# Optimization experiments

Measured on AMD Instinct MI355X. Metric: run time of the kernel, lower is better.

The kernel has to match this reference:

```python
import jax, jax.numpy as jnp
import numpy as np

B, C, H, W = 512, 256, 7, 7
NS, HS, WS = 16, 14, 14
CK = 128            # key/value channels of the 1x1 convs
REP = 1024          # MLP_HEAD_DIM
IN = 2 * CK * H * W # 12544 = concat(query_value, attended_value) flattened


def setup_inputs() -> dict:
    key = jax.random.key(0)
    ks = jax.random.split(key, 14)
    s = lambda n: 1.0 / np.sqrt(n)
    f32 = jnp.float32
    return {
        "x": jax.random.normal(ks[0], (B, C, H, W), f32),
        "sup_features": jax.random.normal(ks[1], (NS, C, HS, WS), f32),
        # 1x1 conv weights [out_c, in_c] + biases
        "Wqv": jax.random.normal(ks[2], (CK, C), f32) * s(C),
        "bqv": jnp.zeros((CK,), f32),
        "Wqk": jax.random.normal(ks[3], (CK, C), f32) * s(C),
        "bqk": jnp.zeros((CK,), f32),
        "Wsv": jax.random.normal(ks[4], (CK, C), f32) * s(C),
        "bsv": jnp.zeros((CK,), f32),
        "Wsk": jax.random.normal(ks[5], (CK, C), f32) * s(C),
        "bsk": jnp.zeros((CK,), f32),
        # fc layers, torch Linear convention: W [out, in]
        "W6c": jax.random.normal(ks[6], (REP, IN), f32) * s(IN),
        "b6c": jnp.zeros((REP,), f32),
        "W7c": jax.random.normal(ks[7], (REP, REP), f32) * s(REP),
        "b7c": jnp.zeros((REP,), f32),
        "W6r": jax.random.normal(ks[8], (REP, IN), f32) * s(IN),
        "b6r": jnp.zeros((REP,), f32),
        "W7r": jax.random.normal(ks[9], (REP, REP), f32) * s(REP),
        "b7r": jnp.zeros((REP,), f32),
    }


def _conv1x1(w, b, t):
    # 1x1 conv == per-pixel channel mixing
    return jnp.einsum('oc,bchw->bohw', w, t) + b[None, :, None, None]


def reference(x, sup_features, Wqv, bqv, Wqk, bqk, Wsv, bsv, Wsk, bsk,
              W6c, b6c, W7c, b7c, W6r, b6r, W7r, b7r):
    qv = _conv1x1(Wqv, bqv, x)                                          # [B,128,H,W]
    qk = _conv1x1(Wqk, bqk, x).transpose(0, 2, 3, 1).reshape(-1, CK)    # [B*H*W,128]
    sv = _conv1x1(Wsv, bsv, sup_features).transpose(0, 2, 3, 1).reshape(-1, CK)  # [M,128]
    sk = _conv1x1(Wsk, bsk, sup_features).transpose(1, 0, 2, 3).reshape(CK, -1)  # [128,M]
    sim = jax.nn.softmax(qk @ sk, axis=-1)                              # [B*H*W, M] (unscaled, as in source)
    att = (sim @ sv).reshape(B, H, W, CK).transpose(0, 3, 1, 2)         # [B,128,H,W]
    fuse = jnp.concatenate([qv, att], axis=1).reshape(B, -1)            # [B,12544]
    xr = jax.nn.relu(fuse @ W6r.T + b6r)
    xr = jax.nn.relu(xr @ W7r.T + b7r)
    xc = jax.nn.relu(fuse @ W6c.T + b6c)
    xc = jax.nn.relu(xc @ W7c.T + b7c)
    return (xc, xr)
```

## Files before the change

### kernel.cpp

```cpp
#include <hip/hip_runtime.h>
#include <hip/hip_bf16.h>
#include <stdint.h>

typedef short short8 __attribute__((ext_vector_type(8)));
typedef float f32x4 __attribute__((ext_vector_type(4)));
typedef ushort ushort4v __attribute__((ext_vector_type(4)));

#define M_Q   25088
#define M_S   3136
#define IN_   12544
#define LOG2E  1.44269504f
#define SHIFT2 57.7078016f
#define NZ    4
#define FZ    8
#define KSTR  136
#define PSTR  40
#define WSTR  40

__device__ __forceinline__ ushort f2bf(float f) {
  union { float f; uint32_t u; } v; v.f = f;
  uint32_t r = v.u + 0x7fffu + ((v.u >> 16) & 1u);
  return (ushort)(r >> 16);
}
__device__ __forceinline__ ushort f2bf_fast(float f) {
  union { float f; uint32_t u; } v; v.f = f;
  return (ushort)((v.u + 0x8000u) >> 16);
}
__device__ __forceinline__ float bf2f(ushort u) {
  union { uint32_t u; float f; } v; v.u = ((uint32_t)u) << 16;
  return v.f;
}
__device__ __forceinline__ f32x4 mfma16(short8 a, short8 b, f32x4 c) {
  return __builtin_amdgcn_mfma_f32_16x16x32_bf16(a, b, c, 0, 0, 0);
}

__global__ __launch_bounds__(256) void transpose_pack(
    const float* __restrict__ src, ushort* __restrict__ hi, int P) {
  const int b = blockIdx.x;
  const int p0 = blockIdx.y * 49;
  const int w = threadIdx.x >> 6, l = threadIdx.x & 63;
  if (l >= 49) return;
  const int p = p0 + l;
  const float* sb = src + (size_t)b * 256 * P + p;
  const size_t orow = ((size_t)b * P + p) * 256;
  const int ch0 = blockIdx.z * 2;
#pragma unroll
  for (int ch = 0; ch < 2; ++ch) {
    const int c0 = ((ch0 + ch) * 4 + w) * 8;
    short8 h8;
#pragma unroll
    for (int j = 0; j < 8; ++j) h8[j] = (short)f2bf(sb[(size_t)(c0 + j) * P]);
    *(short8*)(hi + orow + c0) = h8;
  }
}

__global__ void pack_w(const float* __restrict__ Wqv, const float* __restrict__ Wqk,
                       const float* __restrict__ bqv, const float* __restrict__ bqk,
                       const float* __restrict__ Wsv, const float* __restrict__ Wsk,
                       const float* __restrict__ bsv, const float* __restrict__ bsk,
                       ushort* __restrict__ Wq_h, float* __restrict__ biasq,
                       ushort* __restrict__ Ws_h, float* __restrict__ biass) {
  int idx = blockIdx.x * 256 + threadIdx.x;
  if (idx < 65536) {
    int n = idx >> 8;
    const float* W = (n < 128) ? (Wqv + n * 256) : (Wqk + (n - 128) * 256);
    Wq_h[idx] = f2bf(W[idx & 255]);
  } else if (idx < 131072) {
    int j = idx - 65536;
    int n = j >> 8;
    const float* W = (n < 128) ? (Wsv + n * 256) : (Wsk + (n - 128) * 256);
    Ws_h[j] = f2bf(W[j & 255]);
  } else if (idx < 131328) {
    int n = idx - 131072;
    biasq[n] = (n < 128) ? bqv[n] : bqk[n - 128];
  } else if (idx < 131584) {
    int n = idx - 131328;
    biass[n] = (n < 128) ? bsv[n] : bsk[n - 128];
  }
}

__global__ __launch_bounds__(256) void pack_w6(
    const float* __restrict__ W6c, const float* __restrict__ W6r,
    ushort* __restrict__ W6p) {
  __shared__ ushort tile[IN_];
  const int n = blockIdx.x;
  const float* src = (n < 1024) ? (W6c + (size_t)n * IN_)
                                : (W6r + (size_t)(n - 1024) * IN_);
  ushort* dst = W6p + (size_t)n * IN_;
#pragma unroll 7
  for (int j = 0; j < 49; ++j) {
    int i = j * 256 + threadIdx.x;
    tile[i] = f2bf(src[i]);
  }
  __syncthreads();
#pragma unroll 7
  for (int j = 0; j < 49; ++j) {
    int o = j * 256 + threadIdx.x;
    int c = o & 255, p = o >> 8;
    dst[o] = tile[c * 49 + p];
  }
}

__global__ void pack_w7(const float* __restrict__ W7c, const float* __restrict__ W7r,
                        ushort* __restrict__ W7p) {
  int idx = blockIdx.x * 256 + threadIdx.x;
  float v = (idx < 1048576) ? W7c[idx] : W7r[idx - 1048576];
  W7p[idx] = f2bf(v);
}

__global__ __launch_bounds__(256) void gemm_conv_q(
    const ushort* __restrict__ Ah, const ushort* __restrict__ Bh,
    const float* __restrict__ bias, ushort* __restrict__ fuse,
    ushort* __restrict__ qk_h) {
  const int lane = threadIdx.x & 63, wv = threadIdx.x >> 6;
  const int r = lane & 15, g = lane >> 4;
  const int row0 = blockIdx.x * 64 + wv * 16;
  const ushort* arh = Ah + (size_t)(row0 + r) * 256 + g * 8;
  f32x4 acc[16];
#pragma unroll
  for (int i = 0; i < 16; ++i) acc[i] = f32x4{0.f, 0.f, 0.f, 0.f};
#pragma unroll
  for (int kc = 0; kc < 8; ++kc) {
    short8 ah = *(const short8*)(arh + kc * 32);
    const ushort* bbh = Bh + r * 256 + kc * 32 + g * 8;
#pragma unroll
    for (int nt = 0; nt < 16; ++nt) {
      short8 bh = *(const short8*)(bbh + nt * 16 * 256);
      acc[nt] = mfma16(ah, bh, acc[nt]);
    }
  }
  const int qr = row0 + g * 4;
#pragma unroll
  for (int nt = 0; nt < 16; ++nt) {
    int n = nt * 16 + r;
    float bs = bias[n];
#pragma unroll
    for (int e = 0; e < 4; ++e) {
      float v = acc[nt][e] + bs;
      int q = qr + e;
      if (nt < 8) {
        int b = q / 49, p = q - b * 49;
        fuse[(size_t)b * IN_ + p * 256 + n] = f2bf(v);
      } else {
        qk_h[(size_t)q * 128 + (n - 128)] = f2bf(v * LOG2E);
      }
    }
  }
}

__global__ __launch_bounds__(256) void gemm_conv_s(
    const ushort* __restrict__ Ah, const ushort* __restrict__ Bh,
    const float* __restrict__ bias, ushort* __restrict__ svT,
    ushort* __restrict__ sk_h) {
  const int lane = threadIdx.x & 63, wv = threadIdx.x >> 6;
  const int r = lane & 15, g = lane >> 4;
  const int row0 = blockIdx.x * 64 + wv * 16;
  const int nb = blockIdx.y;
  const ushort* arh = Ah + (size_t)(row0 + r) * 256 + g * 8;
  f32x4 acc[8];
#pragma unroll
  for (int i = 0; i < 8; ++i) acc[i] = f32x4{0.f, 0.f, 0.f, 0.f};
#pragma unroll
  for (int kc = 0; kc < 8; ++kc) {
    short8 ah = *(const short8*)(arh + kc * 32);
    const ushort* bbh = Bh + (size_t)(nb * 128 + r) * 256 + kc * 32 + g * 8;
#pragma unroll
    for (int nt = 0; nt < 8; ++nt) {
      short8 bh = *(const short8*)(bbh + nt * 16 * 256);
      acc[nt] = mfma16(ah, bh, acc[nt]);
    }
  }
  const int qr = row0 + g * 4;
#pragma unroll
  for (int nt = 0; nt < 8; ++nt) {
    int nl = nt * 16 + r;
    float bs = bias[nb * 128 + nl];
#pragma unroll
    for (int e = 0; e < 4; ++e) {
      float v = acc[nt][e] + bs;
      int k = qr + e;
      if (nb == 0) {
        svT[(size_t)nl * M_S + k] = f2bf(v);
      } else {
        sk_h[(size_t)k * 128 + nl] = f2bf(v);
      }
    }
  }
}

#define LOAD_TILE(T)                                                            \
  do {                                                                          \
    const int kb_ = (T) * 32;                                                   \
    pkh0 = *(const short8*)(Kh + (size_t)(kb_ + row0s) * 128 + c8s * 8);        \
    pkh1 = *(const short8*)(Kh + (size_t)(kb_ + row0s + 16) * 128 + c8s * 8);   \
    pv0  = *(const short8*)(Vt + (size_t)cvs * M_S + kb_ + kc2s * 8);           \
    pv1  = *(const short8*)(Vt + (size_t)(cvs + 64) * M_S + kb_ + kc2s * 8);    \
  } while (0)
#define PUBLISH(B)                                                              \
  do {                                                                          \
    *(short8*)(&khs[B][kloff0]) = pkh0;                                         \
    *(short8*)(&khs[B][kloff1]) = pkh1;                                         \
    *(short8*)(&vvs[B][voff0]) = pv0;                                           \
    *(short8*)(&vvs[B][voff1]) = pv1;                                           \
  } while (0)

__global__ __launch_bounds__(256) void attn_kernel(
    const ushort* __restrict__ Qh, const ushort* __restrict__ Kh,
    const ushort* __restrict__ Vt, float* __restrict__ pnum,
    float* __restrict__ pden) {
  __shared__ ushort khs[2][32 * KSTR];
  __shared__ ushort vvs[2][128 * 32];
  __shared__ ushort plds[4][16 * PSTR];
  const int tid = threadIdx.x;
  const int w = tid >> 6, lane = tid & 63;
  const int r = lane & 15, g = lane >> 4;
  const int q0 = blockIdx.x * 128 + w * 32;
  const int z = blockIdx.y;
  const int t0 = z * 24 + (z < 2 ? z : 2);
  const int tn = 24 + (z < 2 ? 1 : 0);
  ushort* pw = plds[w];

  const int row0s = tid >> 4, c8s = tid & 15;
  const int cvs = tid >> 2, kc2s = tid & 3;
  const int kloff0 = row0s * KSTR + c8s * 8;
  const int kloff1 = (row0s + 16) * KSTR + c8s * 8;
  const int voff0 = cvs * 32 + kc2s * 8;
  const int voff1 = (cvs + 64) * 32 + kc2s * 8;

  short8 aq[2][4];
#pragma unroll
  for (int mt = 0; mt < 2; ++mt)
#pragma unroll
    for (int kc = 0; kc < 4; ++kc)
      aq[mt][kc] = *(const short8*)(Qh + (size_t)(q0 + mt * 16 + r) * 128 + kc * 32 + g * 8);

  f32x4 acc[2][8];
#pragma unroll
  for (int mt = 0; mt < 2; ++mt)
#pragma unroll
    for (int ct = 0; ct < 8; ++ct) acc[mt][ct] = f32x4{0.f, 0.f, 0.f, 0.f};
  float den[2][4];
#pragma unroll
  for (int mt = 0; mt < 2; ++mt)
#pragma unroll
    for (int e = 0; e < 4; ++e) den[mt][e] = 0.f;

  short8 pkh0, pkh1, pv0, pv1;
  LOAD_TILE(t0);
  PUBLISH(0);
  if (tn > 1) LOAD_TILE(t0 + 1);
  __syncthreads();

  for (int i = 0; i < tn; ++i) {
    const int b = i & 1;
    if (i + 1 < tn) {
      PUBLISH(b ^ 1);
      if (i + 2 < tn) LOAD_TILE(t0 + i + 2);
    }
    f32x4 lg[2][2];
#pragma unroll
    for (int kt = 0; kt < 2; ++kt) {
      const int kbase = (kt * 16 + r) * KSTR;
      short8 bh[4];
#pragma unroll
      for (int kc = 0; kc < 4; ++kc)
        bh[kc] = *(const short8*)(&khs[b][kbase + (kc * 4 + g) * 8]);
#pragma unroll
      for (int mt = 0; mt < 2; ++mt) {
        f32x4 c = f32x4{0.f, 0.f, 0.f, 0.f};
#pragma unroll
        for (int kc = 0; kc < 4; ++kc)
          c = mfma16(aq[mt][kc], bh[kc], c);
        lg[mt][kt] = c;
      }
    }
    short8 vf[8];
#pragma unroll
    for (int ct = 0; ct < 8; ++ct)
      vf[ct] = *(const short8*)(&vvs[b][(ct * 16 + r) * 32 + g * 8]);
#pragma unroll
    for (int mt = 0; mt < 2; ++mt) {
#pragma unroll
      for (int kt = 0; kt < 2; ++kt)
#pragma unroll
        for (int e = 0; e < 4; ++e) {
          float p = __builtin_amdgcn_exp2f(lg[mt][kt][e] - SHIFT2);
          den[mt][e] += p;
          pw[(g * 4 + e) * PSTR + kt * 16 + r] = f2bf_fast(p);
        }
      short8 pf = *(const short8*)(pw + r * PSTR + g * 8);
#pragma unroll
      for (int ct = 0; ct < 8; ++ct)
        acc[mt][ct] = mfma16(pf, vf[ct], acc[mt][ct]);
    }
    __syncthreads();
  }

#pragma unroll
  for (int mt = 0; mt < 2; ++mt)
#pragma unroll
    for (int e = 0; e < 4; ++e) {
      float d = den[mt][e];
      d += __shfl_xor(d, 1);
      d += __shfl_xor(d, 2);
      d += __shfl_xor(d, 4);
      d += __shfl_xor(d, 8);
      den[mt][e] = d;
    }
#pragma unroll
  for (int mt = 0; mt < 2; ++mt)
#pragma unroll
    for (int ct = 0; ct < 8; ++ct)
#pragma unroll
      for (int e = 0; e < 4; ++e) {
        int q = q0 + mt * 16 + g * 4 + e;
        int c = ct * 16 + r;
        pnum[((size_t)z * M_Q + q) * 128 + c] = acc[mt][ct][e];
      }
  if (r == 0) {
#pragma unroll
    for (int mt = 0; mt < 2; ++mt)
#pragma unroll
      for (int e = 0; e < 4; ++e)
        pden[(size_t)z * M_Q + q0 + mt * 16 + g * 4 + e] = den[mt][e];
  }
}

__global__ void attn_reduce(const float* __restrict__ pnum, const float* __restrict__ pden,
                            ushort* __restrict__ fuse) {
  int idx = blockIdx.x * 256 + threadIdx.x;
  int q = idx >> 5;
  int c4 = (idx & 31) * 4;
  float4 s = {0.f, 0.f, 0.f, 0.f};
  float d = 0.f;
#pragma unroll
  for (int z = 0; z < NZ; ++z) {
    float4 v = *(const float4*)(pnum + ((size_t)z * M_Q + q) * 128 + c4);
    s.x += v.x; s.y += v.y; s.z += v.z; s.w += v.w;
    d += pden[(size_t)z * M_Q + q];
  }
  float inv = 1.0f / d;
  int b = q / 49, p = q - b * 49;
  ushort4v o;
  o[0] = f2bf(s.x * inv); o[1] = f2bf(s.y * inv);
  o[2] = f2bf(s.z * inv); o[3] = f2bf(s.w * inv);
  *(ushort4v*)(fuse + (size_t)b * IN_ + p * 256 + 128 + c4) = o;
}

__global__ __launch_bounds__(256) void fc6_kernel(
    const ushort* __restrict__ fuse, const ushort* __restrict__ W6p,
    float* __restrict__ part) {
  __shared__ ushort wlds[2][64 * WSTR];
  const int lane = threadIdx.x & 63, wv = threadIdx.x >> 6;
  const int r = lane & 15, g = lane >> 4;
  const int m0 = wv * 128;
  const int kz = blockIdx.x & 7;
  const int nidx = (blockIdx.x >> 3) + 4 * blockIdx.y;
  const int n0 = nidx * 64;
  const int k0 = kz * 1568;

  const int srow = threadIdx.x >> 2;
  const int skc  = (threadIdx.x & 3) * 8;
  const size_t wgbase = (size_t)(n0 + srow) * IN_ + k0 + skc;
  const int wloff = srow * WSTR + skc;

  f32x4 acc[8][4];
#pragma unroll
  for (int mt = 0; mt < 8; ++mt)
#pragma unroll
    for (int nt = 0; nt < 4; ++nt) acc[mt][nt] = f32x4{0.f, 0.f, 0.f, 0.f};

  short8 rA, rB;
  rA = *(const short8*)(W6p + wgbase);
  *(short8*)(&wlds[0][wloff]) = rA;
  rA = *(const short8*)(W6p + wgbase + 32);
  rB = *(const short8*)(W6p + wgbase + 64);
  __syncthreads();

  for (int t = 0; t < 49; ++t) {
    const int b = t & 1;
    if (t + 1 < 49) {
      *(short8*)(&wlds[b ^ 1][wloff]) = rA;
      rA = rB;
      if (t + 3 < 49) rB = *(const short8*)(W6p + wgbase + (size_t)(t + 3) * 32);
    }
    const int kcol = k0 + t * 32 + g * 8;
    short8 af[8];
#pragma unroll
    for (int mt = 0; mt < 8; ++mt)
      af[mt] = *(const short8*)(fuse + (size_t)(m0 + mt * 16 + r) * IN_ + kcol);
    short8 bfr[4];
#pragma unroll
    for (int nt = 0; nt < 4; ++nt)
      bfr[nt] = *(const short8*)(&wlds[b][(nt * 16 + r) * WSTR + g * 8]);
#pragma unroll
    for (int mt = 0; mt < 8; ++mt)
#pragma unroll
      for (int nt = 0; nt < 4; ++nt) acc[mt][nt] = mfma16(af[mt], bfr[nt], acc[mt][nt]);
    __syncthreads();
  }
#pragma unroll
  for (int mt = 0; mt < 8; ++mt)
#pragma unroll
    for (int nt = 0; nt < 4; ++nt)
#pragma unroll
      for (int e = 0; e < 4; ++e) {
        int m = m0 + mt * 16 + g * 4 + e;
        int n = n0 + nt * 16 + r;
        part[(size_t)kz * 1048576 + (size_t)m * 2048 + n] = acc[mt][nt][e];
      }
}

__global__ void fc6_reduce(const float* __restrict__ part, const float* __restrict__ b6c,
                           const float* __restrict__ b6r, ushort* __restrict__ X7) {
  int idx = blockIdx.x * 256 + threadIdx.x;
  int n = idx & 2047;
  float s = 0.f;
#pragma unroll
  for (int z = 0; z < FZ; ++z) s += part[(size_t)z * 1048576 + idx];
  s += (n < 1024) ? b6c[n] : b6r[n - 1024];
  s = fmaxf(s, 0.f);
  X7[idx] = f2bf(s);
}

__global__ __launch_bounds__(128) void fc7_kernel(
    const ushort* __restrict__ X7, const ushort* __restrict__ W7p,
    const float* __restrict__ b7c, const float* __restrict__ b7r,
    float* __restrict__ out) {
  const int lane = threadIdx.x & 63, wv = threadIdx.x >> 6;
  const int r = lane & 15, g = lane >> 4;
  const int m0 = blockIdx.x * 32 + wv * 16;
  const int n0 = blockIdx.y * 32;
  const int half = (n0 >= 1024) ? 1 : 0;
  const int nn0 = n0 - half * 1024;
  const float* b7 = half ? b7r : b7c;
  f32x4 acc[2];
#pragma unroll
  for (int nt = 0; nt < 2; ++nt) acc[nt] = f32x4{0.f, 0.f, 0.f, 0.f};
  const ushort* arow = X7 + (size_t)(m0 + r) * 2048 + half * 1024;
  for (int kk = 0; kk < 1024; kk += 32) {
    short8 a = *(const short8*)(arow + kk + g * 8);
#pragma unroll
    for (int nt = 0; nt < 2; ++nt) {
      short8 bb = *(const short8*)(W7p + (size_t)(half * 1024 + nn0 + nt * 16 + r) * 1024 + kk + g * 8);
      acc[nt] = mfma16(a, bb, acc[nt]);
    }
  }
  float* obase = out + (size_t)half * 524288;
#pragma unroll
  for (int nt = 0; nt < 2; ++nt) {
#pragma unroll
    for (int e = 0; e < 4; ++e) {
      int m = m0 + g * 4 + e;
      int n = nn0 + nt * 16 + r;
      obase[(size_t)m * 1024 + n] = fmaxf(acc[nt][e] + b7[n], 0.f);
    }
  }
}

extern "C" void kernel_launch(void* const* d_in, const int* in_sizes, int n_in,
                              void* d_out, int out_size, void* d_ws, size_t ws_size,
                              hipStream_t stream) {
  const float* x    = (const float*)d_in[0];
  const float* sup  = (const float*)d_in[1];
  const float* Wqv  = (const float*)d_in[2];
  const float* bqv  = (const float*)d_in[3];
  const float* Wqk  = (const float*)d_in[4];
  const float* bqk  = (const float*)d_in[5];
  const float* Wsv  = (const float*)d_in[6];
  const float* bsv  = (const float*)d_in[7];
  const float* Wsk  = (const float*)d_in[8];
  const float* bsk  = (const float*)d_in[9];
  const float* W6c  = (const float*)d_in[10];
  const float* b6c  = (const float*)d_in[11];
  const float* W7c  = (const float*)d_in[12];
  const float* b7c  = (const float*)d_in[13];
  const float* W6r  = (const float*)d_in[14];
  const float* b6r  = (const float*)d_in[15];
  const float* W7r  = (const float*)d_in[16];
  const float* b7r  = (const float*)d_in[17];
  float* out = (float*)d_out;

  char* base = (char*)d_ws;
  size_t off = 0;
  auto alloc = [&](size_t bytes) {
    char* p = base + off;
    off += (bytes + 255) & ~(size_t)255;
    return p;
  };
  char* regionA = alloc((size_t)2048 * IN_ * 2 + (size_t)2048 * 1024 * 2);
  ushort* Xp_h = (ushort*)(regionA);
  ushort* Xs_h = (ushort*)(regionA + 12845056);
  ushort* W6p  = (ushort*)(regionA);
  ushort* W7p  = (ushort*)(regionA + (size_t)2048 * IN_ * 2);
  char* regionB = alloc((size_t)NZ * M_Q * 128 * 4);
  float* pnum = (float*)regionB;
  float* part = (float*)regionB;
  ushort* Wq_h = (ushort*)alloc(65536 * 2);
  ushort* Ws_h = (ushort*)alloc(65536 * 2);
  float*  biasq = (float*)alloc(256 * 4);
  float*  biass = (float*)alloc(256 * 4);
  ushort* fuse = (ushort*)alloc((size_t)512 * IN_ * 2);
  ushort* qk_h = (ushort*)alloc((size_t)M_Q * 128 * 2);
  ushort* sk_h = (ushort*)alloc((size_t)M_S * 128 * 2);
  ushort* svT  = (ushort*)alloc((size_t)M_S * 128 * 2);
  float*  pden = (float*)alloc((size_t)NZ * M_Q * 4);
  ushort* X7   = (ushort*)alloc((size_t)512 * 2048 * 2);
  if (off > ws_size) return;

  transpose_pack<<<dim3(512, 1, 4), dim3(256), 0, stream>>>(x, Xp_h, 49);
  transpose_pack<<<dim3(16, 4, 4), dim3(256), 0, stream>>>(sup, Xs_h, 196);
  pack_w<<<dim3(515), dim3(256), 0, stream>>>(Wqv, Wqk, bqv, bqk, Wsv, Wsk, bsv, bsk,
                                              Wq_h, biasq, Ws_h, biass);
  gemm_conv_q<<<dim3(392), dim3(256), 0, stream>>>(Xp_h, Wq_h, biasq, fuse, qk_h);
  gemm_conv_s<<<dim3(49, 2), dim3(256), 0, stream>>>(Xs_h, Ws_h, biass, svT, sk_h);
  pack_w6<<<dim3(2048), dim3(256), 0, stream>>>(W6c, W6r, W6p);
  pack_w7<<<dim3(8192), dim3(256), 0, stream>>>(W7c, W7r, W7p);
  attn_kernel<<<dim3(196, NZ), dim3(256), 0, stream>>>(qk_h, sk_h, svT, pnum, pden);
  attn_reduce<<<dim3(3136), dim3(256), 0, stream>>>(pnum, pden, fuse);
  fc6_kernel<<<dim3(32, FZ), dim3(256), 0, stream>>>(fuse, W6p, part);
  fc6_reduce<<<dim3(4096), dim3(256), 0, stream>>>(part, b6c, b6r, X7);
  fc7_kernel<<<dim3(16, 64), dim3(128), 0, stream>>>(X7, W7p, b7c, b7r, out);
}
```

Measured before the change: 287.9 us.

## Fuse input transposes and W6 packing into GEMM loads

Removes the separate transpose_pack kernels and the pack_w6 kernel. The conv GEMMs now gather fp32 NCHW inputs directly with a 49/196 stride and convert them to bf16 in registers. fc6 reads fp32 W6 rows with the channel/pixel permutation applied on the fly and converts them before staging into LDS. This drops the extra write-then-read of the packed intermediates and the extra launches, but it replaces coalesced reads with strided gathers whose cache lines are poorly reused. For W6 in particular, the working set is large enough that many lines may be fetched more than once.

```diff
diff --git a/kernel.cpp b/kernel.cpp
--- a/kernel.cpp
+++ b/kernel.cpp
@@ -32,26 +32,6 @@
 }
 __device__ __forceinline__ f32x4 mfma16(short8 a, short8 b, f32x4 c) {
   return __builtin_amdgcn_mfma_f32_16x16x32_bf16(a, b, c, 0, 0, 0);
-}
-
-__global__ __launch_bounds__(256) void transpose_pack(
-    const float* __restrict__ src, ushort* __restrict__ hi, int P) {
-  const int b = blockIdx.x;
-  const int p0 = blockIdx.y * 49;
-  const int w = threadIdx.x >> 6, l = threadIdx.x & 63;
-  if (l >= 49) return;
-  const int p = p0 + l;
-  const float* sb = src + (size_t)b * 256 * P + p;
-  const size_t orow = ((size_t)b * P + p) * 256;
-  const int ch0 = blockIdx.z * 2;
-#pragma unroll
-  for (int ch = 0; ch < 2; ++ch) {
-    const int c0 = ((ch0 + ch) * 4 + w) * 8;
-    short8 h8;
-#pragma unroll
-    for (int j = 0; j < 8; ++j) h8[j] = (short)f2bf(sb[(size_t)(c0 + j) * P]);
-    *(short8*)(hi + orow + c0) = h8;
-  }
 }
 
 __global__ void pack_w(const float* __restrict__ Wqv, const float* __restrict__ Wqk,
@@ -79,28 +59,6 @@
   }
 }
 
-__global__ __launch_bounds__(256) void pack_w6(
-    const float* __restrict__ W6c, const float* __restrict__ W6r,
-    ushort* __restrict__ W6p) {
-  __shared__ ushort tile[IN_];
-  const int n = blockIdx.x;
-  const float* src = (n < 1024) ? (W6c + (size_t)n * IN_)
-                                : (W6r + (size_t)(n - 1024) * IN_);
-  ushort* dst = W6p + (size_t)n * IN_;
-#pragma unroll 7
-  for (int j = 0; j < 49; ++j) {
-    int i = j * 256 + threadIdx.x;
-    tile[i] = f2bf(src[i]);
-  }
-  __syncthreads();
-#pragma unroll 7
-  for (int j = 0; j < 49; ++j) {
-    int o = j * 256 + threadIdx.x;
-    int c = o & 255, p = o >> 8;
-    dst[o] = tile[c * 49 + p];
-  }
-}
-
 __global__ void pack_w7(const float* __restrict__ W7c, const float* __restrict__ W7r,
                         ushort* __restrict__ W7p) {
   int idx = blockIdx.x * 256 + threadIdx.x;
@@ -109,19 +67,24 @@
 }
 
 __global__ __launch_bounds__(256) void gemm_conv_q(
-    const ushort* __restrict__ Ah, const ushort* __restrict__ Bh,
+    const float* __restrict__ x, const ushort* __restrict__ Bh,
     const float* __restrict__ bias, ushort* __restrict__ fuse,
     ushort* __restrict__ qk_h) {
   const int lane = threadIdx.x & 63, wv = threadIdx.x >> 6;
   const int r = lane & 15, g = lane >> 4;
   const int row0 = blockIdx.x * 64 + wv * 16;
-  const ushort* arh = Ah + (size_t)(row0 + r) * 256 + g * 8;
+  const int q = row0 + r;
+  const int b = q / 49, p = q - b * 49;
+  const float* xb = x + (size_t)b * IN_ + p;
   f32x4 acc[16];
 #pragma unroll
   for (int i = 0; i < 16; ++i) acc[i] = f32x4{0.f, 0.f, 0.f, 0.f};
 #pragma unroll
   for (int kc = 0; kc < 8; ++kc) {
-    short8 ah = *(const short8*)(arh + kc * 32);
+    const float* s = xb + (size_t)(kc * 32 + g * 8) * 49;
+    short8 ah;
+#pragma unroll
+    for (int j = 0; j < 8; ++j) ah[j] = (short)f2bf(s[(size_t)j * 49]);
     const ushort* bbh = Bh + r * 256 + kc * 32 + g * 8;
 #pragma unroll
     for (int nt = 0; nt < 16; ++nt) {
@@ -137,32 +100,37 @@
 #pragma unroll
     for (int e = 0; e < 4; ++e) {
       float v = acc[nt][e] + bs;
-      int q = qr + e;
+      int qq = qr + e;
       if (nt < 8) {
-        int b = q / 49, p = q - b * 49;
-        fuse[(size_t)b * IN_ + p * 256 + n] = f2bf(v);
+        int bb = qq / 49, pp = qq - bb * 49;
+        fuse[(size_t)bb * IN_ + pp * 256 + n] = f2bf(v);
       } else {
-        qk_h[(size_t)q * 128 + (n - 128)] = f2bf(v * LOG2E);
+        qk_h[(size_t)qq * 128 + (n - 128)] = f2bf(v * LOG2E);
       }
     }
   }
 }
 
 __global__ __launch_bounds__(256) void gemm_conv_s(
-    const ushort* __restrict__ Ah, const ushort* __restrict__ Bh,
+    const float* __restrict__ sup, const ushort* __restrict__ Bh,
     const float* __restrict__ bias, ushort* __restrict__ svT,
     ushort* __restrict__ sk_h) {
   const int lane = threadIdx.x & 63, wv = threadIdx.x >> 6;
   const int r = lane & 15, g = lane >> 4;
   const int row0 = blockIdx.x * 64 + wv * 16;
   const int nb = blockIdx.y;
-  const ushort* arh = Ah + (size_t)(row0 + r) * 256 + g * 8;
+  const int q = row0 + r;
+  const int b = q / 196, p = q - b * 196;
+  const float* xb = sup + (size_t)b * 256 * 196 + p;
   f32x4 acc[8];
 #pragma unroll
   for (int i = 0; i < 8; ++i) acc[i] = f32x4{0.f, 0.f, 0.f, 0.f};
 #pragma unroll
   for (int kc = 0; kc < 8; ++kc) {
-    short8 ah = *(const short8*)(arh + kc * 32);
+    const float* s = xb + (size_t)(kc * 32 + g * 8) * 196;
+    short8 ah;
+#pragma unroll
+    for (int j = 0; j < 8; ++j) ah[j] = (short)f2bf(s[(size_t)j * 196]);
     const ushort* bbh = Bh + (size_t)(nb * 128 + r) * 256 + kc * 32 + g * 8;
 #pragma unroll
     for (int nt = 0; nt < 8; ++nt) {
@@ -348,8 +316,8 @@
 }
 
 __global__ __launch_bounds__(256) void fc6_kernel(
-    const ushort* __restrict__ fuse, const ushort* __restrict__ W6p,
-    float* __restrict__ part) {
+    const ushort* __restrict__ fuse, const float* __restrict__ W6c,
+    const float* __restrict__ W6r, float* __restrict__ part) {
   __shared__ ushort wlds[2][64 * WSTR];
   const int lane = threadIdx.x & 63, wv = threadIdx.x >> 6;
   const int r = lane & 15, g = lane >> 4;
@@ -361,7 +329,9 @@
 
   const int srow = threadIdx.x >> 2;
   const int skc  = (threadIdx.x & 3) * 8;
-  const size_t wgbase = (size_t)(n0 + srow) * IN_ + k0 + skc;
+  const int nrow = n0 + srow;
+  const float* wsrc = (nrow < 1024) ? (W6c + (size_t)nrow * IN_)
+                                    : (W6r + (size_t)(nrow - 1024) * IN_);
   const int wloff = srow * WSTR + skc;
 
   f32x4 acc[8][4];
@@ -370,19 +340,35 @@
 #pragma unroll
     for (int nt = 0; nt < 4; ++nt) acc[mt][nt] = f32x4{0.f, 0.f, 0.f, 0.f};
 
-  short8 rA, rB;
-  rA = *(const short8*)(W6p + wgbase);
-  *(short8*)(&wlds[0][wloff]) = rA;
-  rA = *(const short8*)(W6p + wgbase + 32);
-  rB = *(const short8*)(W6p + wgbase + 64);
+  float rA[8], rB[8];
+#define LOADW(T, dst)                                                           \
+  do {                                                                          \
+    int kk_ = k0 + (T) * 32 + skc;                                              \
+    const float* s_ = wsrc + (kk_ & 255) * 49 + (kk_ >> 8);                     \
+    _Pragma("unroll")                                                           \
+    for (int j_ = 0; j_ < 8; ++j_) dst[j_] = s_[(size_t)j_ * 49];               \
+  } while (0)
+#define CVT8(src, dst)                                                          \
+  do {                                                                          \
+    short8 v_;                                                                  \
+    _Pragma("unroll")                                                           \
+    for (int j_ = 0; j_ < 8; ++j_) v_[j_] = (short)f2bf(src[j_]);               \
+    *(short8*)(dst) = v_;                                                       \
+  } while (0)
+
+  LOADW(0, rA);
+  CVT8(rA, &wlds[0][wloff]);
+  LOADW(1, rA);
+  LOADW(2, rB);
   __syncthreads();
 
   for (int t = 0; t < 49; ++t) {
     const int b = t & 1;
     if (t + 1 < 49) {
-      *(short8*)(&wlds[b ^ 1][wloff]) = rA;
-      rA = rB;
-      if (t + 3 < 49) rB = *(const short8*)(W6p + wgbase + (size_t)(t + 3) * 32);
+      CVT8(rA, &wlds[b ^ 1][wloff]);
+#pragma unroll
+      for (int j = 0; j < 8; ++j) rA[j] = rB[j];
+      if (t + 3 < 49) LOADW(t + 3, rB);
     }
     const int kcol = k0 + t * 32 + g * 8;
     short8 af[8];
@@ -488,14 +474,10 @@
     off += (bytes + 255) & ~(size_t)255;
     return p;
   };
-  char* regionA = alloc((size_t)2048 * IN_ * 2 + (size_t)2048 * 1024 * 2);
-  ushort* Xp_h = (ushort*)(regionA);
-  ushort* Xs_h = (ushort*)(regionA + 12845056);
-  ushort* W6p  = (ushort*)(regionA);
-  ushort* W7p  = (ushort*)(regionA + (size_t)2048 * IN_ * 2);
   char* regionB = alloc((size_t)NZ * M_Q * 128 * 4);
   float* pnum = (float*)regionB;
   float* part = (float*)regionB;
+  ushort* W7p  = (ushort*)alloc((size_t)2048 * 1024 * 2);
   ushort* Wq_h = (ushort*)alloc(65536 * 2);
   ushort* Ws_h = (ushort*)alloc(65536 * 2);
   float*  biasq = (float*)alloc(256 * 4);
@@ -508,17 +490,14 @@
   ushort* X7   = (ushort*)alloc((size_t)512 * 2048 * 2);
   if (off > ws_size) return;
 
-  transpose_pack<<<dim3(512, 1, 4), dim3(256), 0, stream>>>(x, Xp_h, 49);
-  transpose_pack<<<dim3(16, 4, 4), dim3(256), 0, stream>>>(sup, Xs_h, 196);
   pack_w<<<dim3(515), dim3(256), 0, stream>>>(Wqv, Wqk, bqv, bqk, Wsv, Wsk, bsv, bsk,
                                               Wq_h, biasq, Ws_h, biass);
-  gemm_conv_q<<<dim3(392), dim3(256), 0, stream>>>(Xp_h, Wq_h, biasq, fuse, qk_h);
-  gemm_conv_s<<<dim3(49, 2), dim3(256), 0, stream>>>(Xs_h, Ws_h, biass, svT, sk_h);
-  pack_w6<<<dim3(2048), dim3(256), 0, stream>>>(W6c, W6r, W6p);
   pack_w7<<<dim3(8192), dim3(256), 0, stream>>>(W7c, W7r, W7p);
+  gemm_conv_q<<<dim3(392), dim3(256), 0, stream>>>(x, Wq_h, biasq, fuse, qk_h);
+  gemm_conv_s<<<dim3(49, 2), dim3(256), 0, stream>>>(sup, Ws_h, biass, svT, sk_h);
   attn_kernel<<<dim3(196, NZ), dim3(256), 0, stream>>>(qk_h, sk_h, svT, pnum, pden);
   attn_reduce<<<dim3(3136), dim3(256), 0, stream>>>(pnum, pden, fuse);
-  fc6_kernel<<<dim3(32, FZ), dim3(256), 0, stream>>>(fuse, W6p, part);
+  fc6_kernel<<<dim3(32, FZ), dim3(256), 0, stream>>>(fuse, W6c, W6r, part);
   fc6_reduce<<<dim3(4096), dim3(256), 0, stream>>>(part, b6c, b6r, X7);
   fc7_kernel<<<dim3(16, 64), dim3(128), 0, stream>>>(X7, W7p, b7c, b7r, out);
 }
```

Measured after the change: 654.3 us. +127.3%, slower.
